# Kernel optimization log

Measured on AMD Instinct MI355X. Metric: run time of the kernel, lower is better.

Reference implementation:

```python
import jax, jax.numpy as jnp
import numpy as np

SIZE = 512
HEADS = 4
DK = SIZE // HEADS
CHUNK = 16
SHIFT = 8
EPS = 1e-12


def layer_norm(x, g, b):
    m = jnp.mean(x, axis=-1, keepdims=True)
    v = jnp.var(x, axis=-1, keepdims=True)
    return (x - m) / jnp.sqrt(v + EPS) * g + b


def setup_inputs() -> dict:
    key = jax.random.key(0)
    ks = jax.random.split(key, 8)
    B, L, C = 16, 2048, SIZE
    p = lambda k, shp: jax.random.normal(k, shp, jnp.float32) * 0.02
    return {
        "x": jax.random.normal(ks[0], (B, L, C), jnp.float32),
        "mask": jnp.ones((B, 1, L), jnp.float32),
        "pos_emb": jnp.zeros((1, L, C), jnp.float32),
        "mask_pad": jnp.ones((B, 1, L), jnp.float32),
        "Wq": p(ks[1], (C, C)), "bq": jnp.zeros((C,), jnp.float32),
        "Wk": p(ks[2], (C, C)), "bk": jnp.zeros((C,), jnp.float32),
        "Wv": p(ks[3], (C, C)), "bv": jnp.zeros((C,), jnp.float32),
        "Wo": p(ks[4], (C, C)), "bo": jnp.zeros((C,), jnp.float32),
        "g1": jnp.ones((C,), jnp.float32), "be1": jnp.zeros((C,), jnp.float32),
        "g2": jnp.ones((C,), jnp.float32), "be2": jnp.zeros((C,), jnp.float32),
        "W1": p(ks[5], (C, 4 * C)), "bf1": jnp.zeros((4 * C,), jnp.float32),
        "W2": p(ks[6], (4 * C, C)), "bf2": jnp.zeros((C,), jnp.float32),
    }


def reference(x, mask, pos_emb, mask_pad, Wq, bq, Wk, bk, Wv, bv, Wo, bo,
              g1, be1, g2, be2, W1, bf1, W2, bf2):
    B, L, C = x.shape
    nW = L // CHUNK
    half = CHUNK // 2
    # shifted-window attention mask, built exactly as in the torch code
    # (zeros base, -100 in the cross-shift blocks); shape (nW, CHUNK, CHUNK)
    am = jnp.zeros((nW, CHUNK, CHUNK), x.dtype)
    am = am.at[:-1, :half - 1, half:].set(-100.0)
    am = am.at[-1, half:, half:].set(-100.0)

    residual = x
    xn = layer_norm(x, g1, be1)  # normalize_before

    # cyclic shift
    sx = jnp.roll(xn, -SHIFT, axis=1)                    # (B, L, C)
    sm = jnp.roll(mask_pad[:, 0, :], -SHIFT, axis=1)     # (B, L)

    # chunk partition
    xc = sx.reshape(B, nW, CHUNK, C)
    mc = sm.reshape(B, nW, CHUNK)

    # windowed multi-head attention
    q = (xc @ Wq + bq).reshape(B, nW, CHUNK, HEADS, DK)
    k = (xc @ Wk + bk).reshape(B, nW, CHUNK, HEADS, DK)
    v = (xc @ Wv + bv).reshape(B, nW, CHUNK, HEADS, DK)
    scores = jnp.einsum('bwqhd,bwkhd->bwhqk', q, k) / jnp.sqrt(jnp.asarray(DK, x.dtype))
    scores = scores + am[None, :, None]                  # add shift mask per chunk
    valid = mc[:, :, None, None, :] > 0.0                # key padding mask
    scores = jnp.where(valid, scores, jnp.asarray(-1e30, x.dtype))
    attn = jax.nn.softmax(scores, axis=-1)
    attn = jnp.where(valid, attn, jnp.asarray(0.0, x.dtype))
    out = jnp.einsum('bwhqk,bwkhd->bwqhd', attn, v).reshape(B, nW, CHUNK, C)
    out = out @ Wo + bo

    # chunk reverse + reverse shift
    sx_out = out.reshape(B, L, C)
    xa = jnp.roll(sx_out, SHIFT, axis=1)
    m = jnp.roll(sm, SHIFT, axis=1)
    xa = xa * m[:, :, None]
    x1 = residual + xa  # dropout_rate = 0

    # feed forward block (pre-norm, ReLU FFN)
    residual2 = x1
    xn2 = layer_norm(x1, g2, be2)
    h = jax.nn.relu(xn2 @ W1 + bf1)
    x2 = residual2 + (h @ W2 + bf2)
    return x2
```

## Files before the change

### kernel.cpp

```cpp
#include <hip/hip_runtime.h>
#include <stdint.h>


typedef unsigned short bfu;

using bf16x8 = __attribute__((ext_vector_type(8))) __bf16;
using f32x4  = __attribute__((ext_vector_type(4))) float;

union U8 { uint4 v; unsigned short s[8]; };
union F4 { float4 v; float f[4]; };
union ABFrag { uint4 u; bf16x8 f; };

__device__ __forceinline__ float bf2f(unsigned short u) {
    union { uint32_t i; float f; } c; c.i = ((uint32_t)u) << 16; return c.f;
}
__device__ __forceinline__ unsigned short f2bf(float f) {
    union { float f; uint32_t i; } c; c.f = f;
    uint32_t x = c.i;
    return (unsigned short)((x + 0x7FFFu + ((x >> 16) & 1u)) >> 16);
}
__device__ __forceinline__ uint4 pack8(float4 a, float4 b) {
    U8 o;
    o.s[0] = f2bf(a.x); o.s[1] = f2bf(a.y); o.s[2] = f2bf(a.z); o.s[3] = f2bf(a.w);
    o.s[4] = f2bf(b.x); o.s[5] = f2bf(b.y); o.s[6] = f2bf(b.z); o.s[7] = f2bf(b.w);
    return o.v;
}

#define GLDS16(gp, lp)                                                        \
    __builtin_amdgcn_global_load_lds(                                         \
        (__attribute__((address_space(1))) void*)(gp),                        \
        (__attribute__((address_space(3))) void*)(lp), 16, 0, 0)


__global__ __launch_bounds__(256) void wconv_kernel(
    const float* __restrict__ W, bfu* __restrict__ Wt, int K, int N)
{
    __shared__ float t[32][33];
    const int bn = blockIdx.x << 5;
    const int bk = blockIdx.y << 5;
    const int tx = threadIdx.x & 31, ty = threadIdx.x >> 5;
#pragma unroll
    for (int i = 0; i < 32; i += 8)
        t[ty + i][tx] = W[(size_t)(bk + ty + i) * N + bn + tx];
    __syncthreads();
#pragma unroll
    for (int i = 0; i < 32; i += 8)
        Wt[(size_t)(bn + ty + i) * K + bk + tx] = f2bf(t[tx][ty + i]);
}

__global__ __launch_bounds__(256) void wconv3_kernel(
    const float* __restrict__ Wq, const float* __restrict__ Wk,
    const float* __restrict__ Wv, bfu* __restrict__ Wt)
{
    __shared__ float t[32][33];
    const int z = blockIdx.z;
    const float* W = (z == 0) ? Wq : (z == 1) ? Wk : Wv;
    bfu* Wo = Wt + (size_t)z * 512 * 512;
    const int bn = blockIdx.x << 5;
    const int bk = blockIdx.y << 5;
    const int tx = threadIdx.x & 31, ty = threadIdx.x >> 5;
#pragma unroll
    for (int i = 0; i < 32; i += 8)
        t[ty + i][tx] = W[(size_t)(bk + ty + i) * 512 + bn + tx];
    __syncthreads();
#pragma unroll
    for (int i = 0; i < 32; i += 8)
        Wo[(size_t)(bn + ty + i) * 512 + bk + tx] = f2bf(t[tx][ty + i]);
}

__global__ __launch_bounds__(256) void bias_concat_kernel(
    const float* __restrict__ a, const float* __restrict__ b,
    const float* __restrict__ c, float* __restrict__ o)
{
    const int t = blockIdx.x * 256 + threadIdx.x;
    const float* src = (t < 512) ? a : (t < 1024) ? b : c;
    o[t] = src[t & 511];
}


__global__ __launch_bounds__(256) void ln1_shift_kernel(
    const float* __restrict__ x, const float* __restrict__ g,
    const float* __restrict__ be, bfu* __restrict__ out)
{
    const int ms = (blockIdx.x << 2) + (threadIdx.x >> 6);
    const int b = ms >> 11;
    const int ls = ms & 2047;
    const int l = (ls + 8) & 2047;
    const int c0 = (threadIdx.x & 63) << 3;
    const float* xp = x + ((((size_t)(b << 11)) + l) << 9) + c0;
    F4 f0, f1; f0.v = *(const float4*)xp; f1.v = *(const float4*)(xp + 4);
    float vv[8]; float s = 0.f, sq = 0.f;
#pragma unroll
    for (int j = 0; j < 4; ++j) { vv[j] = f0.f[j]; vv[4 + j] = f1.f[j]; }
#pragma unroll
    for (int j = 0; j < 8; ++j) { s += vv[j]; sq += vv[j] * vv[j]; }
#pragma unroll
    for (int o = 32; o > 0; o >>= 1) { s += __shfl_xor(s, o); sq += __shfl_xor(sq, o); }
    const float mean = s * (1.f / 512.f);
    float var = sq * (1.f / 512.f) - mean * mean;
    var = fmaxf(var, 0.f);
    const float rstd = rsqrtf(var + 1e-12f);
    F4 g0, g1v, b0, b1;
    g0.v = *(const float4*)(g + c0);  g1v.v = *(const float4*)(g + c0 + 4);
    b0.v = *(const float4*)(be + c0); b1.v = *(const float4*)(be + c0 + 4);
    U8 o8;
#pragma unroll
    for (int j = 0; j < 4; ++j) {
        o8.s[j]     = f2bf((vv[j]     - mean) * rstd * g0.f[j]  + b0.f[j]);
        o8.s[4 + j] = f2bf((vv[4 + j] - mean) * rstd * g1v.f[j] + b1.f[j]);
    }
    *(uint4*)(out + (((size_t)ms) << 9) + c0) = o8.v;
}

__global__ __launch_bounds__(256) void ln2_kernel(
    const bfu* __restrict__ x1, const float* __restrict__ g,
    const float* __restrict__ be, bfu* __restrict__ out)
{
    const int ms = (blockIdx.x << 2) + (threadIdx.x >> 6);
    const int c0 = (threadIdx.x & 63) << 3;
    U8 u; u.v = *(const uint4*)(x1 + (((size_t)ms) << 9) + c0);
    float vv[8]; float s = 0.f, sq = 0.f;
#pragma unroll
    for (int j = 0; j < 8; ++j) { float f = bf2f(u.s[j]); vv[j] = f; s += f; sq += f * f; }
#pragma unroll
    for (int o = 32; o > 0; o >>= 1) { s += __shfl_xor(s, o); sq += __shfl_xor(sq, o); }
    const float mean = s * (1.f / 512.f);
    float var = sq * (1.f / 512.f) - mean * mean;
    var = fmaxf(var, 0.f);
    const float rstd = rsqrtf(var + 1e-12f);
    F4 g0, g1v, b0, b1;
    g0.v = *(const float4*)(g + c0);  g1v.v = *(const float4*)(g + c0 + 4);
    b0.v = *(const float4*)(be + c0); b1.v = *(const float4*)(be + c0 + 4);
    U8 o8;
#pragma unroll
    for (int j = 0; j < 4; ++j) {
        o8.s[j]     = f2bf((vv[j]     - mean) * rstd * g0.f[j]  + b0.f[j]);
        o8.s[4 + j] = f2bf((vv[4 + j] - mean) * rstd * g1v.f[j] + b1.f[j]);
    }
    *(uint4*)(out + (((size_t)ms) << 9) + c0) = o8.v;
}


template<int EPI>
__global__ __launch_bounds__(512, 4) void mgemm(
    const bfu* __restrict__ X, const bfu* __restrict__ Wt,
    const float* __restrict__ bias,
    bfu* Ob, float* Ofl,
    const float* __restrict__ xres, const bfu* __restrict__ prevb,
    const float* __restrict__ maskpad,
    int M, int N, int K)
{
    __shared__ __align__(16) char smem[49152];
    const char* smc = (const char*)smem;
    float* epi = (float*)smem;

    const int t = threadIdx.x;
    const int lane = t & 63;
    const int w = t >> 6;
    const int wm = w >> 2, wn = w & 3;
    const int q = lane >> 4, l15 = lane & 15;

    const int gx = gridDim.x;
    const int nwg = gx * gridDim.y;
    int wid = blockIdx.y * gx + blockIdx.x;
    wid = ((wid & 7) * (nwg >> 3)) + (wid >> 3);
    const int row0 = (wid / gx) << 7;
    const int col0 = (wid % gx) << 8;

    const int srow = t >> 2;
    const int schunk = (((lane & 3) ^ ((lane >> 3) & 3)) << 3);
    const bfu* gAp  = X  + (size_t)(row0 + srow) * K + schunk;
    const bfu* gB0p = Wt + (size_t)(col0 + srow) * K + schunk;
    const bfu* gB1p = Wt + (size_t)(col0 + 128 + srow) * K + schunk;
    bfu* lsA0  = (bfu*)smem + (t << 3);
    bfu* lsB0  = lsA0 + 4096;
    bfu* lsB0b = lsA0 + 8192;
    bfu* lsA1  = lsA0 + 12288;
    bfu* lsB1  = lsA0 + 16384;
    bfu* lsB1b = lsA0 + 20480;

    const int fswz = (q ^ ((l15 >> 1) & 3)) << 4;
    const int abase = (((wm << 6) + l15) << 6) + fswz;
    const int bbase = 8192 + (((wn << 6) + l15) << 6) + fswz;

    f32x4 acc[4][4];
    float bv[4];
#pragma unroll
    for (int j = 0; j < 4; ++j) bv[j] = bias[col0 + (wn << 6) + (j << 4) + l15];
#pragma unroll
    for (int i = 0; i < 4; ++i)
#pragma unroll
        for (int j = 0; j < 4; ++j) {
            acc[i][j][0] = bv[j]; acc[i][j][1] = bv[j];
            acc[i][j][2] = bv[j]; acc[i][j][3] = bv[j];
        }

    ABFrag a[4], b[4];

#define SB_   __builtin_amdgcn_s_barrier()
#define VM3_  asm volatile("s_waitcnt vmcnt(3)" ::: "memory")
#define VM0_  asm volatile("s_waitcnt vmcnt(0)" ::: "memory")
#define VMNOP_ do {} while (0)

#define LDA_(D)                                                               \
    _Pragma("unroll") for (int mf = 0; mf < 4; ++mf)                          \
        a[mf].u = *(const uint4*)(smc + (D)*24576 + abase + mf*1024);
#define LDB_(D)                                                               \
    _Pragma("unroll") for (int nf = 0; nf < 4; ++nf)                          \
        b[nf].u = *(const uint4*)(smc + (D)*24576 + bbase + nf*1024);
#define MFMAH_(H)                                                             \
    __builtin_amdgcn_s_setprio(1);                                            \
    _Pragma("unroll") for (int mf = 0; mf < 4; ++mf)                          \
    _Pragma("unroll") for (int nf = 2*(H); nf < 2*(H)+2; ++nf)                \
        acc[mf][nf] = __builtin_amdgcn_mfma_f32_16x16x32_bf16(                \
            a[mf].f, b[nf].f, acc[mf][nf], 0, 0, 0);                          \
    __builtin_amdgcn_s_setprio(0);
#define STG3_(D) do {                                                         \
    GLDS16(gAp,  lsA##D);                                                     \
    GLDS16(gB0p, lsB##D);                                                     \
    GLDS16(gB1p, lsB##D##b);                                                  \
    gAp += 32; gB0p += 32; gB1p += 32; } while (0)
#define TILE_(D, DOSTG, VMW) do {                                             \
    SB_;                                                                      \
    LDA_(D); LDB_(D);                                                         \
    MFMAH_(0);                                                                \
    SB_;                                                                      \
    if (DOSTG) STG3_(D);                                                      \
    MFMAH_(1);                                                                \
    VMW;                                                                      \
} while (0)

    const int nT = K >> 5;

    STG3_(0);
    STG3_(1);
    VM3_;

#pragma unroll 1
    for (int tt = 0; tt < nT - 2; tt += 2) {
        TILE_(0, true, VM3_);
        TILE_(1, true, VM3_);
    }
    TILE_(0, false, VM0_);
    TILE_(1, false, VMNOP_);

#undef LDA_
#undef LDB_
#undef MFMAH_
#undef STG3_
#undef TILE_

    SB_;

    float* epw = epi + w * 1088;
    const int c8 = (lane & 7) << 3;
    const int r8 = lane >> 3;
    const int colg = col0 + (wn << 6) + c8;
#pragma unroll
    for (int i = 0; i < 4; ++i) {
#pragma unroll
        for (int j = 0; j < 4; ++j)
#pragma unroll
            for (int r = 0; r < 4; ++r) {
                float y = acc[i][j][r];
                if (EPI == 1) y = fmaxf(y, 0.f);
                epw[((q << 2) + r) * 68 + (j << 4) + l15] = y;
            }
        __builtin_amdgcn_wave_barrier();
#pragma unroll
        for (int h = 0; h < 2; ++h) {
            const int rr = r8 + (h << 3);
            F4 f0, f1;
            f0.v = *(const float4*)&epw[rr * 68 + c8];
            f1.v = *(const float4*)&epw[rr * 68 + c8 + 4];
            const int row_out = row0 + (wm << 6) + (i << 4) + rr;
            if (EPI == 0 || EPI == 1) {
                *(uint4*)(Ob + (size_t)row_out * N + colg) = pack8(f0.v, f1.v);
            } else if (EPI == 2) {
                const int bb2 = row_out >> 11;
                const int ls = row_out & 2047;
                const int l = (ls + 8) & 2047;
                const float mp = maskpad[(bb2 << 11) + l];
                const size_t dst = ((size_t)(bb2 << 11) + l) * (size_t)N + colg;
                F4 x0, x1v;
                x0.v = *(const float4*)(xres + dst);
                x1v.v = *(const float4*)(xres + dst + 4);
                F4 o0, o1;
#pragma unroll
                for (int jj = 0; jj < 4; ++jj) {
                    o0.f[jj] = x0.f[jj]  + f0.f[jj] * mp;
                    o1.f[jj] = x1v.f[jj] + f1.f[jj] * mp;
                }
                *(uint4*)(Ob + dst) = pack8(o0.v, o1.v);
            } else {
                const size_t dst = (size_t)row_out * N + colg;
                U8 pb; pb.v = *(const uint4*)(prevb + dst);
                F4 o0, o1;
#pragma unroll
                for (int jj = 0; jj < 4; ++jj) {
                    o0.f[jj] = bf2f(pb.s[jj])     + f0.f[jj];
                    o1.f[jj] = bf2f(pb.s[4 + jj]) + f1.f[jj];
                }
                *(float4*)(Ofl + dst) = o0.v;
                *(float4*)(Ofl + dst + 4) = o1.v;
            }
        }
        __builtin_amdgcn_wave_barrier();
    }
}


__global__ __launch_bounds__(256) void attn_kernel(
    const bfu* __restrict__ qkv, const float* __restrict__ mpad,
    bfu* __restrict__ out)
{
    __shared__ float qs[16][132];
    __shared__ float ks[16][132];
    __shared__ float vs[16][132];
    __shared__ float ps[16][17];
    const int t = threadIdx.x;
    const int wg = blockIdx.x;
    const int h = blockIdx.y;
    const int b = wg >> 7;
    const int w = wg & 127;
    const int li = t >> 4;
    const int d0 = (t & 15) << 3;
    const size_t bi = (((size_t)wg << 4) + li) * 1536 + (h << 7) + d0;
    U8 uq, uk, uv;
    uq.v = *(const uint4*)(qkv + bi);
    uk.v = *(const uint4*)(qkv + bi + 512);
    uv.v = *(const uint4*)(qkv + bi + 1024);
    F4 a0, a1;
#pragma unroll
    for (int j = 0; j < 4; ++j) { a0.f[j] = bf2f(uq.s[j]); a1.f[j] = bf2f(uq.s[4 + j]); }
    *(float4*)&qs[li][d0] = a0.v;  *(float4*)&qs[li][d0 + 4] = a1.v;
#pragma unroll
    for (int j = 0; j < 4; ++j) { a0.f[j] = bf2f(uk.s[j]); a1.f[j] = bf2f(uk.s[4 + j]); }
    *(float4*)&ks[li][d0] = a0.v;  *(float4*)&ks[li][d0 + 4] = a1.v;
#pragma unroll
    for (int j = 0; j < 4; ++j) { a0.f[j] = bf2f(uv.s[j]); a1.f[j] = bf2f(uv.s[4 + j]); }
    *(float4*)&vs[li][d0] = a0.v;  *(float4*)&vs[li][d0 + 4] = a1.v;
    __syncthreads();
    const int qi = li, ki = t & 15;
    float s = 0.f;
#pragma unroll
    for (int d = 0; d < 128; d += 4) {
        F4 qv, kv;
        qv.v = *(const float4*)&qs[qi][d];
        kv.v = *(const float4*)&ks[ki][d];
        s += qv.f[0] * kv.f[0] + qv.f[1] * kv.f[1]
           + qv.f[2] * kv.f[2] + qv.f[3] * kv.f[3];
    }
    s *= 0.088388347648318447f;
    const bool lastw = (w == 127);
    if (lastw ? (qi >= 8 && ki >= 8) : (qi < 7 && ki >= 8)) s -= 100.f;
    const int lkey = ((w << 4) + ki + 8) & 2047;
    const bool valid = mpad[(b << 11) + lkey] > 0.f;
    if (!valid) s = -1e30f;
    float mx = s;
#pragma unroll
    for (int o = 8; o > 0; o >>= 1) mx = fmaxf(mx, __shfl_xor(mx, o, 16));
    float e = __expf(s - mx);
    float sum = e;
#pragma unroll
    for (int o = 8; o > 0; o >>= 1) sum += __shfl_xor(sum, o, 16);
    float p = e / sum;
    if (!valid) p = 0.f;
    ps[qi][ki] = p;
    __syncthreads();
    F4 o0, o1;
#pragma unroll
    for (int j = 0; j < 4; ++j) { o0.f[j] = 0.f; o1.f[j] = 0.f; }
#pragma unroll
    for (int kk = 0; kk < 16; ++kk) {
        const float pw = ps[li][kk];
        F4 v0, v1;
        v0.v = *(const float4*)&vs[kk][d0];
        v1.v = *(const float4*)&vs[kk][d0 + 4];
#pragma unroll
        for (int j = 0; j < 4; ++j) {
            o0.f[j] += pw * v0.f[j];
            o1.f[j] += pw * v1.f[j];
        }
    }
    U8 o8;
#pragma unroll
    for (int j = 0; j < 4; ++j) { o8.s[j] = f2bf(o0.f[j]); o8.s[4 + j] = f2bf(o1.f[j]); }
    *(uint4*)(out + (((size_t)wg << 4) + li) * 512 + (h << 7) + d0) = o8.v;
}


extern "C" void kernel_launch(void* const* d_in, const int* in_sizes, int n_in,
                              void* d_out, int out_size, void* d_ws, size_t ws_size,
                              hipStream_t stream)
{
    const float* x    = (const float*)d_in[0];
    const float* mpad = (const float*)d_in[3];
    const float* Wq = (const float*)d_in[4];  const float* bq = (const float*)d_in[5];
    const float* Wk = (const float*)d_in[6];  const float* bk = (const float*)d_in[7];
    const float* Wv = (const float*)d_in[8];  const float* bv = (const float*)d_in[9];
    const float* Wo = (const float*)d_in[10]; const float* bo = (const float*)d_in[11];
    const float* g1 = (const float*)d_in[12]; const float* be1 = (const float*)d_in[13];
    const float* g2 = (const float*)d_in[14]; const float* be2 = (const float*)d_in[15];
    const float* W1 = (const float*)d_in[16]; const float* bf1 = (const float*)d_in[17];
    const float* W2 = (const float*)d_in[18]; const float* bf2 = (const float*)d_in[19];
    float* out = (float*)d_out;

    char* p = (char*)d_ws;
    const size_t MB = (size_t)1 << 20;
    bfu* xn_s = (bfu*)p;
    bfu* att  = xn_s;
    bfu* qkv  = (bfu*)(p + 32 * MB);
    bfu* x1   = qkv;
    bfu* W1t  = (bfu*)(p + 64 * MB);
    bfu* W2t  = (bfu*)(p + 66 * MB);
    bfu* xn2  = (bfu*)(p + 96 * MB);
    bfu* hreg = (bfu*)(p + 128 * MB);
    bfu* Wqkvt = hreg;
    bfu* Wot   = hreg + 1536 * 512;
    float* bqkv = (float*)(hreg + 2048 * 512);

    const int M = 32768;
    dim3 blk(256);
    dim3 blk5(512);

    wconv3_kernel<<<dim3(16, 16, 3), blk, 0, stream>>>(Wq, Wk, Wv, Wqkvt);
    wconv_kernel<<<dim3(16, 16), blk, 0, stream>>>(Wo, Wot, 512, 512);
    bias_concat_kernel<<<dim3(6), blk, 0, stream>>>(bq, bk, bv, bqkv);

    ln1_shift_kernel<<<8192, blk, 0, stream>>>(x, g1, be1, xn_s);

    mgemm<0><<<dim3(6, 256), blk5, 0, stream>>>(xn_s, Wqkvt, bqkv, qkv, nullptr, nullptr, nullptr, nullptr, M, 1536, 512);

    attn_kernel<<<dim3(2048, 4), blk, 0, stream>>>(qkv, mpad, att);

    wconv_kernel<<<dim3(64, 16), blk, 0, stream>>>(W1, W1t, 512, 2048);
    wconv_kernel<<<dim3(16, 64), blk, 0, stream>>>(W2, W2t, 2048, 512);

    mgemm<2><<<dim3(2, 256), blk5, 0, stream>>>(att, Wot, bo, x1, nullptr, x, nullptr, mpad, M, 512, 512);

    ln2_kernel<<<8192, blk, 0, stream>>>(x1, g2, be2, xn2);

    mgemm<1><<<dim3(8, 256), blk5, 0, stream>>>(xn2, W1t, bf1, hreg, nullptr, nullptr, nullptr, nullptr, M, 2048, 512);
    mgemm<3><<<dim3(2, 256), blk5, 0, stream>>>(hreg, W2t, bf2, nullptr, out, nullptr, x1, nullptr, M, 512, 2048);
}
```

Measured before the change: 505.6 us.

## Triple-buffer LDS in GEMM mainloop to prefetch two tiles ahead

Grows the shared-memory staging area from two to three tile buffers and rotates through them in groups of three tiles. Each tile now reads its fragments from LDS before the barrier, then immediately issues the global-to-LDS load for the buffer two tiles ahead. The intent is more distance between loads and their use, and less time spent waiting at barriers. In exchange, shared memory per block rises to 72 KB, which can cut the number of resident blocks per CU, and the loop trip count now assumes (K/32 - 4) is divisible by 3.

```diff
diff --git a/kernel.cpp b/kernel.cpp
--- a/kernel.cpp
+++ b/kernel.cpp
@@ -150,7 +150,7 @@
     const float* __restrict__ maskpad,
     int M, int N, int K)
 {
-    __shared__ __align__(16) char smem[49152];
+    __shared__ __align__(16) char smem[73728];
     const char* smc = (const char*)smem;
     float* epi = (float*)smem;
 
@@ -172,12 +172,7 @@
     const bfu* gAp  = X  + (size_t)(row0 + srow) * K + schunk;
     const bfu* gB0p = Wt + (size_t)(col0 + srow) * K + schunk;
     const bfu* gB1p = Wt + (size_t)(col0 + 128 + srow) * K + schunk;
-    bfu* lsA0  = (bfu*)smem + (t << 3);
-    bfu* lsB0  = lsA0 + 4096;
-    bfu* lsB0b = lsA0 + 8192;
-    bfu* lsA1  = lsA0 + 12288;
-    bfu* lsB1  = lsA0 + 16384;
-    bfu* lsB1b = lsA0 + 20480;
+    bfu* lsA  = (bfu*)smem + (t << 3);
 
     const int fswz = (q ^ ((l15 >> 1) & 3)) << 4;
     const int abase = (((wm << 6) + l15) << 6) + fswz;
@@ -215,19 +210,19 @@
         acc[mf][nf] = __builtin_amdgcn_mfma_f32_16x16x32_bf16(                \
             a[mf].f, b[nf].f, acc[mf][nf], 0, 0, 0);                          \
     __builtin_amdgcn_s_setprio(0);
-#define STG3_(D) do {                                                         \
-    GLDS16(gAp,  lsA##D);                                                     \
-    GLDS16(gB0p, lsB##D);                                                     \
-    GLDS16(gB1p, lsB##D##b);                                                  \
+#define STG3_(BUF) do {                                                       \
+    GLDS16(gAp,  lsA + (BUF)*12288);                                          \
+    GLDS16(gB0p, lsA + (BUF)*12288 + 4096);                                   \
+    GLDS16(gB1p, lsA + (BUF)*12288 + 8192);                                   \
     gAp += 32; gB0p += 32; gB1p += 32; } while (0)
-#define TILE_(D, DOSTG, VMW) do {                                             \
+#define TILE_(D, E, DOSTG, VMW) do {                                          \
+    LDA_(D); LDB_(D);                                                         \
     SB_;                                                                      \
-    LDA_(D); LDB_(D);                                                         \
+    if (DOSTG) STG3_(E);                                                      \
     MFMAH_(0);                                                                \
+    VMW;                                                                      \
     SB_;                                                                      \
-    if (DOSTG) STG3_(D);                                                      \
     MFMAH_(1);                                                                \
-    VMW;                                                                      \
 } while (0)
 
     const int nT = K >> 5;
@@ -235,14 +230,19 @@
     STG3_(0);
     STG3_(1);
     VM3_;
-
+    SB_;
+
+    const int nG = (nT - 4) / 3;
 #pragma unroll 1
-    for (int tt = 0; tt < nT - 2; tt += 2) {
-        TILE_(0, true, VM3_);
-        TILE_(1, true, VM3_);
-    }
-    TILE_(0, false, VM0_);
-    TILE_(1, false, VMNOP_);
+    for (int g = 0; g < nG; ++g) {
+        TILE_(0, 2, true, VM3_);
+        TILE_(1, 0, true, VM3_);
+        TILE_(2, 1, true, VM3_);
+    }
+    TILE_(0, 2, true, VM3_);
+    TILE_(1, 0, true, VM3_);
+    TILE_(2, 1, false, VM0_);
+    TILE_(0, 2, false, VMNOP_);
 
 #undef LDA_
 #undef LDB_
```

Measured after the change: 637.0 us. 26.0% more time.
